# Kernel optimization log

Hardware: AMD Instinct MI355X
Metric: run time of the kernel (lower is better)

The kernel has to match this reference:

```python
import jax, jax.numpy as jnp
import numpy as np

N, E = 50000, 800000
F_N, F_E = 32, 16
HC, H, C, L = 128, 2, 64, 3  # hidden_channels, heads, out per head, num_layers
NEG_SLOPE = 0.2  # PyG GATConv default


def setup_inputs() -> dict:
    key = jax.random.key(0)
    ks = jax.random.split(key, 32)
    rn = lambda k, shape, s=0.05: (jax.random.normal(k, shape, jnp.float32) * s)
    return {
        "x": jax.random.normal(ks[0], (N, F_N), jnp.float32),
        "edge_index": jax.random.randint(ks[1], (2, E), 0, N),
        "edge_attr": jax.random.normal(ks[2], (E, F_E), jnp.float32),
        # node encoder: Linear(32,128) -> ReLU -> Linear(128,128)
        "w_n1": rn(ks[3], (F_N, HC)), "b_n1": jnp.zeros((HC,), jnp.float32),
        "w_n2": rn(ks[4], (HC, HC)), "b_n2": jnp.zeros((HC,), jnp.float32),
        # edge encoder: Linear(16,128) -> ReLU (output is ignored by GATConv, edge_dim=None)
        "w_e": rn(ks[5], (F_E, HC)), "b_e": jnp.zeros((HC,), jnp.float32),
        # 3 GATConv layers: lin [128,H*C], att_src/att_dst [H,C], bias [H*C]
        "conv_w": rn(ks[6], (L, HC, H * C)),
        "conv_att_src": rn(ks[7], (L, H, C)),
        "conv_att_dst": rn(ks[8], (L, H, C)),
        "conv_b": jnp.zeros((L, H * C), jnp.float32),
        # path prediction head: Linear(256,128)->ReLU->Linear(128,64)->ReLU->Linear(64,1)->Sigmoid
        "wp1": rn(ks[9], (2 * HC, HC)), "bp1": jnp.zeros((HC,), jnp.float32),
        "wp2": rn(ks[10], (HC, 64)), "bp2": jnp.zeros((64,), jnp.float32),
        "wp3": rn(ks[11], (64, 1)), "bp3": jnp.zeros((1,), jnp.float32),
        # vulnerability head: Linear(128,64)->ReLU->Linear(64,1)->Sigmoid
        "wv1": rn(ks[12], (HC, 64)), "bv1": jnp.zeros((64,), jnp.float32),
        "wv2": rn(ks[13], (64, 1)), "bv2": jnp.zeros((1,), jnp.float32),
    }


def _gat_layer(x, src, dst, w, att_src, att_dst, bias):
    n = x.shape[0]
    h = (x @ w).reshape(n, H, C)                       # [N,H,C]
    a_src = jnp.sum(h * att_src, axis=-1)              # [N,H]
    a_dst = jnp.sum(h * att_dst, axis=-1)              # [N,H]
    alpha = a_src[src] + a_dst[dst]                    # [E',H]
    alpha = jax.nn.leaky_relu(alpha, NEG_SLOPE)
    amax = jax.lax.stop_gradient(jax.ops.segment_max(alpha, dst, num_segments=n))
    ex = jnp.exp(alpha - amax[dst])
    denom = jax.ops.segment_sum(ex, dst, num_segments=n)  # [N,H] (>0: self-loops)
    coef = ex / denom[dst]                             # softmax over incoming edges
    msg = h[src] * coef[:, :, None]                    # [E',H,C]
    out = jax.ops.segment_sum(msg, dst, num_segments=n)
    return out.reshape(n, H * C) + bias


def reference(x, edge_index, edge_attr,
              w_n1, b_n1, w_n2, b_n2, w_e, b_e,
              conv_w, conv_att_src, conv_att_dst, conv_b,
              wp1, bp1, wp2, bp2, wp3, bp3, wv1, bv1, wv2, bv2):
    n = x.shape[0]
    # node encoder (dropout = identity in eval)
    h = jax.nn.relu(x @ w_n1 + b_n1) @ w_n2 + b_n2
    # edge encoder output is computed but ignored by GATConv (edge_dim=None in PyG)
    _edge_emb = jax.nn.relu(edge_attr @ w_e + b_e)
    # add self loops (GATConv default add_self_loops=True)
    loop = jnp.arange(n, dtype=edge_index.dtype)
    src = jnp.concatenate([edge_index[0], loop])
    dst = jnp.concatenate([edge_index[1], loop])
    for l in range(L):
        h = jax.nn.relu(_gat_layer(h, src, dst, conv_w[l], conv_att_src[l], conv_att_dst[l], conv_b[l]))
    g = jnp.mean(h, axis=0, keepdims=True)             # [1,128] graph embedding
    # path head on cat(x[:1], graph_embedding)
    p = jnp.concatenate([h[:1], g], axis=1)            # [1,256]
    p = jax.nn.relu(p @ wp1 + bp1)
    p = jax.nn.relu(p @ wp2 + bp2)
    path = jax.nn.sigmoid(p @ wp3 + bp3)               # [1,1]
    v = jax.nn.relu(h @ wv1 + bv1)
    vuln = jax.nn.sigmoid(v @ wv2 + bv2)               # [N,1]
    esc = jnp.zeros((1, 1), jnp.float32)               # [1,1]
    return (path, vuln, esc)
```

## Files before the change

kernel.cpp:

```cpp
#include <hip/hip_runtime.h>
#include <math.h>

#define HC 128
#define NSLOPE 0.2f

using bf16x8 = __attribute__((ext_vector_type(8))) short;
using f32x4  = __attribute__((ext_vector_type(4))) float;

__device__ __forceinline__ float lrelu(float v){ return v > 0.f ? v : NSLOPE * v; }

__device__ __forceinline__ unsigned short f2bf(float f){
    unsigned int b = __float_as_uint(f);
    b += 0x7FFFu + ((b >> 16) & 1u);
    return (unsigned short)(b >> 16);
}
__device__ __forceinline__ float bf_lo(unsigned int v){ return __uint_as_float(v << 16); }
__device__ __forceinline__ float bf_hi(unsigned int v){ return __uint_as_float(v & 0xFFFF0000u); }
__device__ __forceinline__ float bf1(unsigned short v){ return __uint_as_float((unsigned int)v << 16); }

__global__ void count_kernel(const int* __restrict__ ei, int* __restrict__ cnt,
                             int* __restrict__ rank, int E){
    int e = blockIdx.x * blockDim.x + threadIdx.x;
    if (e < E) rank[e] = atomicAdd(&cnt[ei[E + e]], 1);
}

__global__ __launch_bounds__(256) void scan_part_kernel(
        const int* __restrict__ deg, int* __restrict__ bsum, int n)
{
    int t = threadIdx.x, lane = t & 63, wid = t >> 6;
    int base = blockIdx.x * 1024 + t * 4;
    int s = 0;
    #pragma unroll
    for (int j = 0; j < 4; ++j){ int i = base + j; if (i < n) s += deg[i]; }
    #pragma unroll
    for (int o = 1; o < 64; o <<= 1) s += __shfl_xor(s, o);
    __shared__ int red[4];
    if (lane == 0) red[wid] = s;
    __syncthreads();
    if (t == 0) bsum[blockIdx.x] = red[0] + red[1] + red[2] + red[3];
}

__global__ __launch_bounds__(64) void scan_top_kernel(
        const int* __restrict__ bsum, int* __restrict__ boff, int* __restrict__ rowptr,
        int nb, int n)
{
    int t = threadIdx.x;
    int v = (t < nb) ? bsum[t] : 0;
    int incl = v;
    #pragma unroll
    for (int o = 1; o < 64; o <<= 1){ int u = __shfl_up(incl, o); if (t >= o) incl += u; }
    if (t < nb) boff[t] = incl - v;
    if (t == 63) rowptr[n] = incl;
}

__global__ __launch_bounds__(256) void scan_fin_kernel(
        const int* __restrict__ deg, const int* __restrict__ boff,
        int* __restrict__ rowptr, int n)
{
    int t = threadIdx.x, lane = t & 63, wid = t >> 6;
    int base = blockIdx.x * 1024 + t * 4;
    int d[4]; int s = 0;
    #pragma unroll
    for (int j = 0; j < 4; ++j){ int i = base + j; d[j] = (i < n) ? deg[i] : 0; s += d[j]; }
    int incl = s;
    #pragma unroll
    for (int o = 1; o < 64; o <<= 1){ int u = __shfl_up(incl, o); if (lane >= o) incl += u; }
    __shared__ int wsum[4];
    if (lane == 63) wsum[wid] = incl;
    __syncthreads();
    int off = boff[blockIdx.x] + (incl - s);
    for (int w = 0; w < wid; ++w) off += wsum[w];
    #pragma unroll
    for (int j = 0; j < 4; ++j){
        int i = base + j;
        if (i < n) rowptr[i] = off;
        off += d[j];
    }
}

__global__ __launch_bounds__(256) void scatter_kernel(
        const int* __restrict__ ei, const int* __restrict__ rowptr,
        const int* __restrict__ rank, int* __restrict__ colsrc, int E)
{
    int b = blockIdx.x * 2048 + threadIdx.x;
    int e[8]; bool v[8]; int d[8], s[8], r[8];
    #pragma unroll
    for (int i = 0; i < 8; ++i){ e[i] = b + i * 256; v[i] = e[i] < E; }
    #pragma unroll
    for (int i = 0; i < 8; ++i) if (v[i]){ d[i] = ei[E + e[i]]; s[i] = ei[e[i]]; r[i] = rank[e[i]]; }
    #pragma unroll
    for (int i = 0; i < 8; ++i) if (v[i]) colsrc[rowptr[d[i]] + r[i]] = s[i];
}

__global__ __launch_bounds__(256) void wtrans_kernel(
        const float* __restrict__ W, unsigned short* __restrict__ Wt,
        int K, int C, int nmat)
{
    int kg8 = K >> 3;
    int per = C * kg8;
    int idx = blockIdx.x * 256 + threadIdx.x;
    if (idx >= nmat * per) return;
    int mat = idx / per;
    int rem = idx - mat * per;
    int c = rem / kg8, kg = rem - c * kg8;
    const float* Wm = W + (size_t)mat * K * C;
    unsigned short* Wo = Wt + (size_t)mat * K * C;
    unsigned int pk[4];
    #pragma unroll
    for (int j = 0; j < 4; ++j){
        float a = Wm[(size_t)(kg*8 + j*2    ) * C + c];
        float b = Wm[(size_t)(kg*8 + j*2 + 1) * C + c];
        pk[j] = (unsigned int)f2bf(a) | ((unsigned int)f2bf(b) << 16);
    }
    *(uint4*)(Wo + (size_t)c * K + kg * 8) = make_uint4(pk[0], pk[1], pk[2], pk[3]);
}

__global__ __launch_bounds__(256) void enc1_kernel(
        const float* __restrict__ x, const float* __restrict__ w1, const float* __restrict__ b1,
        unsigned short* __restrict__ hid, int n)
{
    __shared__ float As[32][68];
    __shared__ float Bs[32][128];
    int t = threadIdx.x;
    int m0 = blockIdx.x * 64;
    int tm = t >> 4, tn = t & 15;

    #pragma unroll
    for (int i = 0; i < 2; ++i){
        int f = i * 256 + t;
        int row = f >> 3, kq = f & 7;
        int gr = m0 + row; if (gr > n - 1) gr = n - 1;
        float4 v = *(const float4*)(x + (size_t)gr * 32 + kq * 4);
        As[kq*4+0][row] = v.x; As[kq*4+1][row] = v.y; As[kq*4+2][row] = v.z; As[kq*4+3][row] = v.w;
    }
    #pragma unroll
    for (int i = 0; i < 4; ++i){
        int f = i * 256 + t;
        int kk = f >> 5, nq = f & 31;
        *(float4*)&Bs[kk][nq*4] = *(const float4*)(w1 + (size_t)kk * 128 + nq * 4);
    }
    __syncthreads();

    float acc[4][8];
    #pragma unroll
    for (int i = 0; i < 4; ++i)
        #pragma unroll
        for (int j = 0; j < 8; ++j) acc[i][j] = 0.f;

    #pragma unroll 4
    for (int k = 0; k < 32; ++k){
        float a[4], b[8];
        *(float4*)&a[0] = *(float4*)&As[k][tm*4];
        *(float4*)&b[0] = *(float4*)&Bs[k][tn*8];
        *(float4*)&b[4] = *(float4*)&Bs[k][tn*8+4];
        #pragma unroll
        for (int i = 0; i < 4; ++i)
            #pragma unroll
            for (int j = 0; j < 8; ++j) acc[i][j] = fmaf(a[i], b[j], acc[i][j]);
    }

    float bb[8];
    *(float4*)&bb[0] = *(const float4*)(b1 + tn*8);
    *(float4*)&bb[4] = *(const float4*)(b1 + tn*8 + 4);
    #pragma unroll
    for (int i = 0; i < 4; ++i){
        int node = m0 + tm*4 + i;
        if (node < n){
            float o[8];
            #pragma unroll
            for (int j = 0; j < 8; ++j) o[j] = fmaxf(acc[i][j] + bb[j], 0.f);
            uint4 pk;
            pk.x = (unsigned int)f2bf(o[0]) | ((unsigned int)f2bf(o[1]) << 16);
            pk.y = (unsigned int)f2bf(o[2]) | ((unsigned int)f2bf(o[3]) << 16);
            pk.z = (unsigned int)f2bf(o[4]) | ((unsigned int)f2bf(o[5]) << 16);
            pk.w = (unsigned int)f2bf(o[6]) | ((unsigned int)f2bf(o[7]) << 16);
            *(uint4*)(hid + (size_t)node*HC + tn*8) = pk;
        }
    }
}

template<bool ATT>
__global__ __launch_bounds__(256) void gemm_mfma_kernel(
        const unsigned short* __restrict__ A, const unsigned short* __restrict__ Wt,
        const float* __restrict__ bias,
        const float* __restrict__ att_s, const float* __restrict__ att_d,
        unsigned short* __restrict__ Cb,
        float* __restrict__ asrc, float* __restrict__ adst, int n)
{
    __shared__ float lds[4][16][132];
    int t = threadIdx.x;
    int w = t >> 6, l = t & 63;
    int lane15 = l & 15, lanehi = l >> 4;
    int m0 = blockIdx.x * 64 + w * 16;

    f32x4 acc[8];
    #pragma unroll
    for (int ct = 0; ct < 8; ++ct) acc[ct] = (f32x4){0.f, 0.f, 0.f, 0.f};

    int ar = m0 + lane15; if (ar > n - 1) ar = n - 1;
    const unsigned short* Arow = A + (size_t)ar * HC;

    #pragma unroll
    for (int kc = 0; kc < 4; ++kc){
        bf16x8 af = *reinterpret_cast<const bf16x8*>(Arow + kc * 32 + lanehi * 8);
        #pragma unroll
        for (int ct = 0; ct < 8; ++ct){
            bf16x8 bf = *reinterpret_cast<const bf16x8*>(
                Wt + (size_t)(ct * 16 + lane15) * HC + kc * 32 + lanehi * 8);
            acc[ct] = __builtin_amdgcn_mfma_f32_16x16x32_bf16(af, bf, acc[ct], 0, 0, 0);
        }
    }

    if (ATT){
        float ats[8], atd[8];
        #pragma unroll
        for (int ct = 0; ct < 8; ++ct){
            ats[ct] = att_s[ct * 16 + lane15];
            atd[ct] = att_d[ct * 16 + lane15];
        }
        #pragma unroll
        for (int r = 0; r < 4; ++r){
            float sa0 = 0.f, sd0 = 0.f, sa1 = 0.f, sd1 = 0.f;
            #pragma unroll
            for (int ct = 0; ct < 4; ++ct){
                sa0 = fmaf(acc[ct][r], ats[ct], sa0);
                sd0 = fmaf(acc[ct][r], atd[ct], sd0);
            }
            #pragma unroll
            for (int ct = 4; ct < 8; ++ct){
                sa1 = fmaf(acc[ct][r], ats[ct], sa1);
                sd1 = fmaf(acc[ct][r], atd[ct], sd1);
            }
            #pragma unroll
            for (int o = 1; o < 16; o <<= 1){
                sa0 += __shfl_xor(sa0, o); sd0 += __shfl_xor(sd0, o);
                sa1 += __shfl_xor(sa1, o); sd1 += __shfl_xor(sd1, o);
            }
            int node = m0 + lanehi * 4 + r;
            if (lane15 == 0 && node < n){
                asrc[(size_t)node * 2]     = sa0;
                adst[(size_t)node * 2]     = sd0;
                asrc[(size_t)node * 2 + 1] = sa1;
                adst[(size_t)node * 2 + 1] = sd1;
            }
        }
    }

    float bb[8];
    #pragma unroll
    for (int ct = 0; ct < 8; ++ct) bb[ct] = ATT ? 0.f : bias[ct * 16 + lane15];
    #pragma unroll
    for (int ct = 0; ct < 8; ++ct)
        #pragma unroll
        for (int r = 0; r < 4; ++r)
            lds[w][lanehi * 4 + r][ct * 16 + lane15] = acc[ct][r] + bb[ct];
    __syncthreads();

    int row = lane15, cb = lanehi;
    int node = m0 + row;
    if (node < n){
        #pragma unroll
        for (int q = 0; q < 4; ++q){
            float o[8];
            *(float4*)&o[0] = *(float4*)&lds[w][row][cb * 32 + q * 8];
            *(float4*)&o[4] = *(float4*)&lds[w][row][cb * 32 + q * 8 + 4];
            uint4 pk;
            pk.x = (unsigned int)f2bf(o[0]) | ((unsigned int)f2bf(o[1]) << 16);
            pk.y = (unsigned int)f2bf(o[2]) | ((unsigned int)f2bf(o[3]) << 16);
            pk.z = (unsigned int)f2bf(o[4]) | ((unsigned int)f2bf(o[5]) << 16);
            pk.w = (unsigned int)f2bf(o[6]) | ((unsigned int)f2bf(o[7]) << 16);
            *(uint4*)(Cb + (size_t)node * HC + cb * 32 + q * 8) = pk;
        }
    }
}

__global__ __launch_bounds__(64) void aggregate_kernel(
        const unsigned short* __restrict__ h1b, const float* __restrict__ asrc, const float* __restrict__ adst,
        const int* __restrict__ rowptr, const int* __restrict__ colsrc,
        const float* __restrict__ bias, unsigned short* __restrict__ hout, int n)
{
    __shared__ float4 exl[64];
    int i = blockIdx.x;
    if (i >= n) return;
    int t = threadIdx.x;
    int head = t >> 5;
    float2 adv = *(const float2*)(adst + (size_t)i * 2);
    float2 asv = *(const float2*)(asrc + (size_t)i * 2);
    float ads = head ? adv.y : adv.x;
    float exs = __expf(lrelu((head ? asv.y : asv.x) + ads));
    unsigned int hv = ((const unsigned int*)(h1b + (size_t)i * HC))[t];
    float acc0 = exs * bf_lo(hv), acc1 = exs * bf_hi(hv), D = exs;

    int e  = rowptr[i];
    int e1 = rowptr[i + 1];
    while (e < e1){
        int m = e1 - e; if (m > 64) m = 64;
        if (t < m){
            int s = colsrc[e + t];
            float2 as = *(const float2*)(asrc + (size_t)s * 2);
            exl[t] = make_float4(__int_as_float(s),
                                 __expf(lrelu(as.x + adv.x)),
                                 __expf(lrelu(as.y + adv.y)), 0.f);
        }
        __syncthreads();
        int j = 0;
        for (; j + 8 <= m; j += 8){
            float4 q[8];
            #pragma unroll
            for (int u = 0; u < 8; ++u) q[u] = exl[j + u];
            unsigned int v[8];
            #pragma unroll
            for (int u = 0; u < 8; ++u)
                v[u] = ((const unsigned int*)(h1b + (size_t)__float_as_int(q[u].x) * HC))[t];
            #pragma unroll
            for (int u = 0; u < 8; ++u){
                float c = head ? q[u].z : q[u].y;
                acc0 = fmaf(c, bf_lo(v[u]), acc0);
                acc1 = fmaf(c, bf_hi(v[u]), acc1);
                D += c;
            }
        }
        for (; j < m; ++j){
            float4 q = exl[j];
            unsigned int v = ((const unsigned int*)(h1b + (size_t)__float_as_int(q.x) * HC))[t];
            float c = head ? q.z : q.y;
            acc0 = fmaf(c, bf_lo(v), acc0);
            acc1 = fmaf(c, bf_hi(v), acc1);
            D += c;
        }
        __syncthreads();
        e += m;
    }
    float rD = 1.0f / D;
    float o0 = fmaxf(acc0 * rD + bias[2*t],     0.f);
    float o1 = fmaxf(acc1 * rD + bias[2*t + 1], 0.f);
    ((unsigned int*)hout)[(size_t)i * 64 + t] =
        (unsigned int)f2bf(o0) | ((unsigned int)f2bf(o1) << 16);
}

__global__ __launch_bounds__(256) void mean_part_kernel(
        const unsigned short* __restrict__ h, float* __restrict__ partial, int n)
{
    int t = threadIdx.x;
    int cq = t & 31;
    int rl = t >> 5;
    float4 acc = make_float4(0.f, 0.f, 0.f, 0.f);
    for (int i = blockIdx.x * 8 + rl; i < n; i += gridDim.x * 8){
        uint2 v = *(const uint2*)(h + (size_t)i * HC + cq * 4);
        acc.x += bf_lo(v.x); acc.y += bf_hi(v.x);
        acc.z += bf_lo(v.y); acc.w += bf_hi(v.y);
    }
    __shared__ float4 red[256];
    red[t] = acc;
    __syncthreads();
    if (t < 128){
        float4 o = red[t + 128];
        red[t].x += o.x; red[t].y += o.y; red[t].z += o.z; red[t].w += o.w;
    }
    __syncthreads();
    if (t < 64){
        float4 o = red[t + 64];
        red[t].x += o.x; red[t].y += o.y; red[t].z += o.z; red[t].w += o.w;
    }
    __syncthreads();
    if (t < 32){
        float4 a = red[t], b = red[t + 32];
        float4 s = make_float4(a.x + b.x, a.y + b.y, a.z + b.z, a.w + b.w);
        *(float4*)(partial + (size_t)blockIdx.x * HC + t * 4) = s;
    }
}

__global__ __launch_bounds__(256) void mean_fin_kernel(
        const float* __restrict__ partial, float* __restrict__ g, int nb)
{
    int t = threadIdx.x;
    int cq = t & 31, b0 = t >> 5;
    float4 acc = make_float4(0.f, 0.f, 0.f, 0.f);
    for (int b = b0; b < nb; b += 8){
        float4 v = *(const float4*)(partial + (size_t)b * HC + cq * 4);
        acc.x += v.x; acc.y += v.y; acc.z += v.z; acc.w += v.w;
    }
    __shared__ float4 red[256];
    red[t] = acc;
    __syncthreads();
    if (t < 128){
        float4 o = red[t + 128];
        red[t].x += o.x; red[t].y += o.y; red[t].z += o.z; red[t].w += o.w;
    }
    __syncthreads();
    if (t < 64){
        float4 o = red[t + 64];
        red[t].x += o.x; red[t].y += o.y; red[t].z += o.z; red[t].w += o.w;
    }
    __syncthreads();
    if (t < 32){
        float4 a = red[t], b = red[t + 32];
        float4 s = make_float4(a.x + b.x, a.y + b.y, a.z + b.z, a.w + b.w);
        *(float4*)(g + t * 4) = s;
    }
}

__global__ __launch_bounds__(256) void vuln_mfma_kernel(
        const unsigned short* __restrict__ h, const unsigned short* __restrict__ Wtv,
        const float* __restrict__ bv1, const float* __restrict__ wv2,
        const float* __restrict__ bv2, float* __restrict__ out, int n)
{
    int t = threadIdx.x;
    int w = t >> 6, l = t & 63;
    int lane15 = l & 15, lanehi = l >> 4;
    int m0 = blockIdx.x * 64 + w * 16;

    f32x4 acc[4];
    #pragma unroll
    for (int ct = 0; ct < 4; ++ct) acc[ct] = (f32x4){0.f, 0.f, 0.f, 0.f};

    int ar = m0 + lane15; if (ar > n - 1) ar = n - 1;
    const unsigned short* Arow = h + (size_t)ar * HC;

    #pragma unroll
    for (int kc = 0; kc < 4; ++kc){
        bf16x8 af = *reinterpret_cast<const bf16x8*>(Arow + kc * 32 + lanehi * 8);
        #pragma unroll
        for (int ct = 0; ct < 4; ++ct){
            bf16x8 bf = *reinterpret_cast<const bf16x8*>(
                Wtv + (size_t)(ct * 16 + lane15) * HC + kc * 32 + lanehi * 8);
            acc[ct] = __builtin_amdgcn_mfma_f32_16x16x32_bf16(af, bf, acc[ct], 0, 0, 0);
        }
    }

    float bb[4], wv[4];
    #pragma unroll
    for (int ct = 0; ct < 4; ++ct){
        bb[ct] = bv1[ct * 16 + lane15];
        wv[ct] = wv2[ct * 16 + lane15];
    }
    float bv2v = bv2[0];
    #pragma unroll
    for (int r = 0; r < 4; ++r){
        float s = 0.f;
        #pragma unroll
        for (int ct = 0; ct < 4; ++ct)
            s = fmaf(fmaxf(acc[ct][r] + bb[ct], 0.f), wv[ct], s);
        #pragma unroll
        for (int o = 1; o < 16; o <<= 1) s += __shfl_xor(s, o);
        int node = m0 + lanehi * 4 + r;
        if (lane15 == 0 && node < n)
            out[1 + node] = 1.0f / (1.0f + __expf(-(s + bv2v)));
    }
}

__global__ __launch_bounds__(128) void path_kernel(
        const unsigned short* __restrict__ h, const float* __restrict__ g,
        const float* __restrict__ wp1, const float* __restrict__ bp1,
        const float* __restrict__ wp2, const float* __restrict__ bp2,
        const float* __restrict__ wp3, const float* __restrict__ bp3,
        float* __restrict__ out, int n)
{
    __shared__ float pc[256];
    __shared__ float p1[HC];
    __shared__ float p2[64];
    int t = threadIdx.x;
    pc[t]       = bf1(h[t]);
    pc[128 + t] = g[t] * (1.0f / (float)n);
    __syncthreads();
    float a = bp1[t];
    for (int k = 0; k < 256; ++k) a = fmaf(pc[k], wp1[k * HC + t], a);
    p1[t] = fmaxf(a, 0.f);
    __syncthreads();
    if (t < 64){
        float a2 = bp2[t];
        for (int k = 0; k < HC; ++k) a2 = fmaf(p1[k], wp2[k * 64 + t], a2);
        p2[t] = fmaxf(a2, 0.f);
    }
    __syncthreads();
    if (t == 0){
        float a3 = bp3[0];
        for (int k = 0; k < 64; ++k) a3 = fmaf(p2[k], wp3[k], a3);
        out[0] = 1.0f / (1.0f + __expf(-a3));
        out[1 + n] = 0.f;
    }
}

extern "C" void kernel_launch(void* const* d_in, const int* in_sizes, int n_in,
                              void* d_out, int out_size, void* d_ws, size_t ws_size,
                              hipStream_t stream)
{
    const float* x    = (const float*)d_in[0];
    const int*   ei   = (const int*)d_in[1];
    const float* w_n1 = (const float*)d_in[3];
    const float* b_n1 = (const float*)d_in[4];
    const float* w_n2 = (const float*)d_in[5];
    const float* b_n2 = (const float*)d_in[6];
    const float* conv_w = (const float*)d_in[9];
    const float* att_s  = (const float*)d_in[10];
    const float* att_d  = (const float*)d_in[11];
    const float* conv_b = (const float*)d_in[12];
    const float* wp1 = (const float*)d_in[13];
    const float* bp1 = (const float*)d_in[14];
    const float* wp2 = (const float*)d_in[15];
    const float* bp2 = (const float*)d_in[16];
    const float* wp3 = (const float*)d_in[17];
    const float* bp3 = (const float*)d_in[18];
    const float* wv1 = (const float*)d_in[19];
    const float* bv1 = (const float*)d_in[20];
    const float* wv2 = (const float*)d_in[21];
    const float* bv2 = (const float*)d_in[22];

    const int N = in_sizes[0] / 32;
    const int E = in_sizes[1] / 2;
    float* out = (float*)d_out;

    char* ws = (char*)d_ws;
    size_t off = 0;
    auto take = [&](size_t bytes) -> char* {
        char* p = ws + off;
        off += (bytes + 255) & ~(size_t)255;
        return p;
    };
    unsigned short* hA = (unsigned short*)take((size_t)N * HC * 2);
    unsigned short* hB = (unsigned short*)take((size_t)N * HC * 2);
    float* asrc  = (float*)take((size_t)N * 2 * 4);
    float* adst  = (float*)take((size_t)N * 2 * 4);
    int*   rowptr= (int*)take((size_t)(N + 1) * 4);
    int*   cnt   = (int*)take((size_t)N * 4);
    int*   rank  = (int*)take((size_t)E * 4);
    int*   colsrc= (int*)take((size_t)E * 4);
    float* g     = (float*)take(HC * 4);
    unsigned short* Wt0 = (unsigned short*)take(16384 * 2);
    unsigned short* Wt1 = (unsigned short*)take((size_t)3 * 16384 * 2);
    unsigned short* Wtv = (unsigned short*)take(8192 * 2);
    const int MB = 64;
    float* mpart = (float*)take((size_t)MB * HC * 4);
    int nb = (N + 1023) / 1024;
    int*   bsum  = (int*)take((size_t)((nb + 63) & ~63) * 4);
    int*   boff  = (int*)take((size_t)((nb + 63) & ~63) * 4);

    hipMemsetAsync(cnt, 0, (size_t)N * 4, stream);
    count_kernel<<<(E + 255) / 256, 256, 0, stream>>>(ei, cnt, rank, E);
    scan_part_kernel<<<nb, 256, 0, stream>>>(cnt, bsum, N);
    scan_top_kernel<<<1, 64, 0, stream>>>(bsum, boff, rowptr, nb, N);
    scan_fin_kernel<<<nb, 256, 0, stream>>>(cnt, boff, rowptr, N);
    scatter_kernel<<<(E + 2047) / 2048, 256, 0, stream>>>(ei, rowptr, rank, colsrc, E);

    wtrans_kernel<<<8, 256, 0, stream>>>(w_n2, Wt0, 128, 128, 1);
    wtrans_kernel<<<24, 256, 0, stream>>>(conv_w, Wt1, 128, 128, 3);
    wtrans_kernel<<<4, 256, 0, stream>>>(wv1, Wtv, 128, 64, 1);

    int nblk64 = (N + 63) / 64;
    enc1_kernel<<<nblk64, 256, 0, stream>>>(x, w_n1, b_n1, hB, N);
    gemm_mfma_kernel<false><<<nblk64, 256, 0, stream>>>(
        hB, Wt0, b_n2, nullptr, nullptr, hA, nullptr, nullptr, N);

    for (int l = 0; l < 3; ++l){
        gemm_mfma_kernel<true><<<nblk64, 256, 0, stream>>>(
            hA, Wt1 + (size_t)l * 16384, nullptr,
            att_s + (size_t)l * HC, att_d + (size_t)l * HC,
            hB, asrc, adst, N);
        aggregate_kernel<<<N, 64, 0, stream>>>(
            hB, asrc, adst, rowptr, colsrc, conv_b + (size_t)l * HC, hA, N);
    }

    mean_part_kernel<<<MB, 256, 0, stream>>>(hA, mpart, N);
    mean_fin_kernel<<<1, 256, 0, stream>>>(mpart, g, MB);
    vuln_mfma_kernel<<<nblk64, 256, 0, stream>>>(hA, Wtv, bv1, wv2, bv2, out, N);
    path_kernel<<<1, 128, 0, stream>>>(hA, g, wp1, bp1, wp2, bp2, wp3, bp3, out, N);
}
```

Baseline: 333.9 us.

## Store projected GAT features as fp8 and gather them in a shuffle-based aggregate kernel

The attention GEMM now writes its projected node features as packed fp8 (e4m3) instead of bf16, which halves the bytes the edge-gather in the aggregation kernel has to read. The aggregate kernel broadcasts source indices and exp weights with wave shuffles instead of LDS plus __syncthreads, and packs four nodes (one wave each) per 256-thread block. The three weight-transpose launches are merged into one. Rounding features to fp8 loses precision and may push outputs past tolerance.

```diff
diff --git a/kernel.cpp b/kernel.cpp
--- a/kernel.cpp
+++ b/kernel.cpp
@@ -92,19 +92,21 @@
     for (int i = 0; i < 8; ++i) if (v[i]) colsrc[rowptr[d[i]] + r[i]] = s[i];
 }
 
-__global__ __launch_bounds__(256) void wtrans_kernel(
-        const float* __restrict__ W, unsigned short* __restrict__ Wt,
-        int K, int C, int nmat)
-{
-    int kg8 = K >> 3;
-    int per = C * kg8;
+__global__ __launch_bounds__(256) void wtrans_all_kernel(
+        const float* __restrict__ w_n2, const float* __restrict__ conv_w,
+        const float* __restrict__ wv1,
+        unsigned short* __restrict__ Wt0, unsigned short* __restrict__ Wt1,
+        unsigned short* __restrict__ Wtv)
+{
     int idx = blockIdx.x * 256 + threadIdx.x;
-    if (idx >= nmat * per) return;
-    int mat = idx / per;
-    int rem = idx - mat * per;
-    int c = rem / kg8, kg = rem - c * kg8;
-    const float* Wm = W + (size_t)mat * K * C;
-    unsigned short* Wo = Wt + (size_t)mat * K * C;
+    if (idx >= 9216) return;
+    const float* Wm; unsigned short* Wo; int C; int rem;
+    if (idx < 2048){ Wm = w_n2; Wo = Wt0; C = 128; rem = idx; }
+    else if (idx < 8192){
+        int m2 = (idx - 2048) >> 11; rem = (idx - 2048) & 2047;
+        Wm = conv_w + (size_t)m2 * 16384; Wo = Wt1 + (size_t)m2 * 16384; C = 128;
+    } else { rem = idx - 8192; Wm = wv1; Wo = Wtv; C = 64; }
+    int c = rem >> 4, kg = rem & 15;
     unsigned int pk[4];
     #pragma unroll
     for (int j = 0; j < 4; ++j){
@@ -112,7 +114,7 @@
         float b = Wm[(size_t)(kg*8 + j*2 + 1) * C + c];
         pk[j] = (unsigned int)f2bf(a) | ((unsigned int)f2bf(b) << 16);
     }
-    *(uint4*)(Wo + (size_t)c * K + kg * 8) = make_uint4(pk[0], pk[1], pk[2], pk[3]);
+    *(uint4*)(Wo + (size_t)c * 128 + kg * 8) = make_uint4(pk[0], pk[1], pk[2], pk[3]);
 }
 
 __global__ __launch_bounds__(256) void enc1_kernel(
@@ -184,7 +186,7 @@
         const unsigned short* __restrict__ A, const unsigned short* __restrict__ Wt,
         const float* __restrict__ bias,
         const float* __restrict__ att_s, const float* __restrict__ att_d,
-        unsigned short* __restrict__ Cb,
+        unsigned short* __restrict__ Cb, unsigned char* __restrict__ C8,
         float* __restrict__ asrc, float* __restrict__ adst, int n)
 {
     __shared__ float lds[4][16][132];
@@ -259,76 +261,94 @@
     int row = lane15, cb = lanehi;
     int node = m0 + row;
     if (node < n){
-        #pragma unroll
-        for (int q = 0; q < 4; ++q){
-            float o[8];
-            *(float4*)&o[0] = *(float4*)&lds[w][row][cb * 32 + q * 8];
-            *(float4*)&o[4] = *(float4*)&lds[w][row][cb * 32 + q * 8 + 4];
-            uint4 pk;
-            pk.x = (unsigned int)f2bf(o[0]) | ((unsigned int)f2bf(o[1]) << 16);
-            pk.y = (unsigned int)f2bf(o[2]) | ((unsigned int)f2bf(o[3]) << 16);
-            pk.z = (unsigned int)f2bf(o[4]) | ((unsigned int)f2bf(o[5]) << 16);
-            pk.w = (unsigned int)f2bf(o[6]) | ((unsigned int)f2bf(o[7]) << 16);
-            *(uint4*)(Cb + (size_t)node * HC + cb * 32 + q * 8) = pk;
-        }
-    }
-}
-
-__global__ __launch_bounds__(64) void aggregate_kernel(
-        const unsigned short* __restrict__ h1b, const float* __restrict__ asrc, const float* __restrict__ adst,
+        if (!ATT){
+            #pragma unroll
+            for (int q = 0; q < 4; ++q){
+                float o[8];
+                *(float4*)&o[0] = *(float4*)&lds[w][row][cb * 32 + q * 8];
+                *(float4*)&o[4] = *(float4*)&lds[w][row][cb * 32 + q * 8 + 4];
+                uint4 pk;
+                pk.x = (unsigned int)f2bf(o[0]) | ((unsigned int)f2bf(o[1]) << 16);
+                pk.y = (unsigned int)f2bf(o[2]) | ((unsigned int)f2bf(o[3]) << 16);
+                pk.z = (unsigned int)f2bf(o[4]) | ((unsigned int)f2bf(o[5]) << 16);
+                pk.w = (unsigned int)f2bf(o[6]) | ((unsigned int)f2bf(o[7]) << 16);
+                *(uint4*)(Cb + (size_t)node * HC + cb * 32 + q * 8) = pk;
+            }
+        } else {
+            unsigned int words[8];
+            #pragma unroll
+            for (int gq = 0; gq < 8; ++gq){
+                float4 v = *(float4*)&lds[w][row][cb * 32 + gq * 4];
+                unsigned int r = __builtin_amdgcn_cvt_pk_fp8_f32(v.x, v.y, 0, 0);
+                r = __builtin_amdgcn_cvt_pk_fp8_f32(v.z, v.w, r, 1);
+                words[gq] = r;
+            }
+            *(uint4*)(C8 + (size_t)node * HC + cb * 32)      = make_uint4(words[0], words[1], words[2], words[3]);
+            *(uint4*)(C8 + (size_t)node * HC + cb * 32 + 16) = make_uint4(words[4], words[5], words[6], words[7]);
+        }
+    }
+}
+
+__global__ __launch_bounds__(256) void aggregate_kernel(
+        const unsigned char* __restrict__ h8, const float* __restrict__ asrc,
+        const float* __restrict__ adst,
         const int* __restrict__ rowptr, const int* __restrict__ colsrc,
         const float* __restrict__ bias, unsigned short* __restrict__ hout, int n)
 {
-    __shared__ float4 exl[64];
-    int i = blockIdx.x;
+    int i = blockIdx.x * 4 + (threadIdx.x >> 6);
     if (i >= n) return;
-    int t = threadIdx.x;
+    int t = threadIdx.x & 63;
     int head = t >> 5;
     float2 adv = *(const float2*)(adst + (size_t)i * 2);
     float2 asv = *(const float2*)(asrc + (size_t)i * 2);
     float ads = head ? adv.y : adv.x;
     float exs = __expf(lrelu((head ? asv.y : asv.x) + ads));
-    unsigned int hv = ((const unsigned int*)(h1b + (size_t)i * HC))[t];
-    float acc0 = exs * bf_lo(hv), acc1 = exs * bf_hi(hv), D = exs;
+    unsigned int hv = *(const unsigned short*)(h8 + (size_t)i * HC + t * 2);
+    float acc0 = exs * __builtin_amdgcn_cvt_f32_fp8(hv, 0);
+    float acc1 = exs * __builtin_amdgcn_cvt_f32_fp8(hv, 1);
+    float D = exs;
 
     int e  = rowptr[i];
     int e1 = rowptr[i + 1];
     while (e < e1){
         int m = e1 - e; if (m > 64) m = 64;
+        int sl = 0; float ex0 = 0.f, ex1 = 0.f;
         if (t < m){
-            int s = colsrc[e + t];
-            float2 as = *(const float2*)(asrc + (size_t)s * 2);
-            exl[t] = make_float4(__int_as_float(s),
-                                 __expf(lrelu(as.x + adv.x)),
-                                 __expf(lrelu(as.y + adv.y)), 0.f);
-        }
-        __syncthreads();
+            sl = colsrc[e + t];
+            float2 as = *(const float2*)(asrc + (size_t)sl * 2);
+            ex0 = __expf(lrelu(as.x + adv.x));
+            ex1 = __expf(lrelu(as.y + adv.y));
+        }
         int j = 0;
         for (; j + 8 <= m; j += 8){
-            float4 q[8];
-            #pragma unroll
-            for (int u = 0; u < 8; ++u) q[u] = exl[j + u];
+            int s[8]; float c[8];
+            #pragma unroll
+            for (int u = 0; u < 8; ++u){
+                s[u] = __shfl(sl, j + u);
+                float c0 = __shfl(ex0, j + u);
+                float c1 = __shfl(ex1, j + u);
+                c[u] = head ? c1 : c0;
+            }
             unsigned int v[8];
             #pragma unroll
             for (int u = 0; u < 8; ++u)
-                v[u] = ((const unsigned int*)(h1b + (size_t)__float_as_int(q[u].x) * HC))[t];
+                v[u] = *(const unsigned short*)(h8 + (size_t)s[u] * HC + t * 2);
             #pragma unroll
             for (int u = 0; u < 8; ++u){
-                float c = head ? q[u].z : q[u].y;
-                acc0 = fmaf(c, bf_lo(v[u]), acc0);
-                acc1 = fmaf(c, bf_hi(v[u]), acc1);
-                D += c;
+                acc0 = fmaf(c[u], __builtin_amdgcn_cvt_f32_fp8(v[u], 0), acc0);
+                acc1 = fmaf(c[u], __builtin_amdgcn_cvt_f32_fp8(v[u], 1), acc1);
+                D += c[u];
             }
         }
         for (; j < m; ++j){
-            float4 q = exl[j];
-            unsigned int v = ((const unsigned int*)(h1b + (size_t)__float_as_int(q.x) * HC))[t];
-            float c = head ? q.z : q.y;
-            acc0 = fmaf(c, bf_lo(v), acc0);
-            acc1 = fmaf(c, bf_hi(v), acc1);
+            int s = __shfl(sl, j);
+            float c0 = __shfl(ex0, j), c1 = __shfl(ex1, j);
+            float c = head ? c1 : c0;
+            unsigned int v = *(const unsigned short*)(h8 + (size_t)s * HC + t * 2);
+            acc0 = fmaf(c, __builtin_amdgcn_cvt_f32_fp8(v, 0), acc0);
+            acc1 = fmaf(c, __builtin_amdgcn_cvt_f32_fp8(v, 1), acc1);
             D += c;
         }
-        __syncthreads();
         e += m;
     }
     float rD = 1.0f / D;
@@ -519,6 +539,7 @@
     };
     unsigned short* hA = (unsigned short*)take((size_t)N * HC * 2);
     unsigned short* hB = (unsigned short*)take((size_t)N * HC * 2);
+    unsigned char*  h8 = (unsigned char*)take((size_t)N * HC);
     float* asrc  = (float*)take((size_t)N * 2 * 4);
     float* adst  = (float*)take((size_t)N * 2 * 4);
     int*   rowptr= (int*)take((size_t)(N + 1) * 4);
@@ -542,22 +563,20 @@
     scan_fin_kernel<<<nb, 256, 0, stream>>>(cnt, boff, rowptr, N);
     scatter_kernel<<<(E + 2047) / 2048, 256, 0, stream>>>(ei, rowptr, rank, colsrc, E);
 
-    wtrans_kernel<<<8, 256, 0, stream>>>(w_n2, Wt0, 128, 128, 1);
-    wtrans_kernel<<<24, 256, 0, stream>>>(conv_w, Wt1, 128, 128, 3);
-    wtrans_kernel<<<4, 256, 0, stream>>>(wv1, Wtv, 128, 64, 1);
+    wtrans_all_kernel<<<36, 256, 0, stream>>>(w_n2, conv_w, wv1, Wt0, Wt1, Wtv);
 
     int nblk64 = (N + 63) / 64;
     enc1_kernel<<<nblk64, 256, 0, stream>>>(x, w_n1, b_n1, hB, N);
     gemm_mfma_kernel<false><<<nblk64, 256, 0, stream>>>(
-        hB, Wt0, b_n2, nullptr, nullptr, hA, nullptr, nullptr, N);
+        hB, Wt0, b_n2, nullptr, nullptr, hA, nullptr, nullptr, nullptr, N);
 
     for (int l = 0; l < 3; ++l){
         gemm_mfma_kernel<true><<<nblk64, 256, 0, stream>>>(
             hA, Wt1 + (size_t)l * 16384, nullptr,
             att_s + (size_t)l * HC, att_d + (size_t)l * HC,
-            hB, asrc, adst, N);
-        aggregate_kernel<<<N, 64, 0, stream>>>(
-            hB, asrc, adst, rowptr, colsrc, conv_b + (size_t)l * HC, hA, N);
+            nullptr, h8, asrc, adst, N);
+        aggregate_kernel<<<(N + 3) / 4, 256, 0, stream>>>(
+            h8, asrc, adst, rowptr, colsrc, conv_b + (size_t)l * HC, hA, N);
     }
 
     mean_part_kernel<<<MB, 256, 0, stream>>>(hA, mpart, N);
```

After: 325.4 us. -2.6%, faster.
